# Kernel tuning notes

Measured on AMD Instinct MI355X. Metric: run time of the kernel, lower is better.

The kernel has to match this reference:

```python
import jax, jax.numpy as jnp
import numpy as np

V, C, T, H, L, B = 32000, 1024, 1024, 16, 8, 4
HS = C // H
STD = 0.02


def _layernorm(x, g, b, eps=1e-5):
    m = jnp.mean(x, axis=-1, keepdims=True)
    v = jnp.mean(jnp.square(x - m), axis=-1, keepdims=True)
    return (x - m) * jax.lax.rsqrt(v + eps) * g + b


def setup_inputs() -> dict:
    key = jax.random.key(0)
    ks = jax.random.split(key, 16)
    n = lambda k, shape: (jax.random.normal(k, shape, dtype=jnp.float32) * STD)
    return {
        "index": jax.random.randint(ks[0], (B, T), 0, V),
        "targets": jax.random.randint(ks[1], (B, T), 0, V),
        "tok_emb": n(ks[2], (V, C)),
        "pos_emb": n(ks[3], (T, C)),
        "wq": n(ks[4], (L, C, C)),
        "wk": n(ks[5], (L, C, C)),
        "wv": n(ks[6], (L, C, C)),
        "wo": n(ks[7], (L, C, C)),
        "bo": jnp.zeros((L, C), jnp.float32),
        "w1": n(ks[8], (L, C, 4 * C)),
        "b1": jnp.zeros((L, 4 * C), jnp.float32),
        "w2": n(ks[9], (L, 4 * C, C)),
        "b2": jnp.zeros((L, C), jnp.float32),
        "ln1_g": jnp.ones((L, C), jnp.float32),
        "ln1_b": jnp.zeros((L, C), jnp.float32),
        "ln2_g": jnp.ones((L, C), jnp.float32),
        "ln2_b": jnp.zeros((L, C), jnp.float32),
        "lnf_g": jnp.ones((C,), jnp.float32),
        "lnf_b": jnp.zeros((C,), jnp.float32),
        "lm_w": n(ks[10], (C, V)),
        "lm_b": jnp.zeros((V,), jnp.float32),
    }


def reference(index, targets, tok_emb, pos_emb, wq, wk, wv, wo, bo, w1, b1, w2,
              b2, ln1_g, ln1_b, ln2_g, ln2_b, lnf_g, lnf_b, lm_w, lm_b):
    b, t = index.shape
    x = tok_emb[index] + pos_emb[:t]                      # [B,T,C]
    causal = jnp.tril(jnp.ones((t, t), dtype=bool))       # tril mask
    scale = HS ** -0.5
    for l in range(L):  # fixed small layer loop
        q = (x @ wq[l]).reshape(b, t, H, HS)
        k = (x @ wk[l]).reshape(b, t, H, HS)
        v = (x @ wv[l]).reshape(b, t, H, HS)
        scores = jnp.einsum('bqhd,bkhd->bhqk', q, k) * scale
        scores = jnp.where(causal, scores, -jnp.inf)
        w = jax.nn.softmax(scores, axis=-1)               # dropout p=0 -> identity
        att = jnp.einsum('bhqk,bkhd->bqhd', w, v).reshape(b, t, C)
        x = _layernorm(x + att @ wo[l] + bo[l], ln1_g[l], ln1_b[l])
        h = jax.nn.relu(x @ w1[l] + b1[l])
        x = _layernorm(x + h @ w2[l] + b2[l], ln2_g[l], ln2_b[l])
    x = _layernorm(x, lnf_g, lnf_b)
    logits = (x @ lm_w + lm_b).reshape(b * t, V)
    logp = jax.nn.log_softmax(logits, axis=-1)
    loss = -jnp.take_along_axis(logp, targets.reshape(-1, 1), axis=1).mean()
    return logits, loss
```

## Files before the change

kernel.cpp:

```cpp
#include <hip/hip_runtime.h>

typedef unsigned short u16;
typedef __attribute__((ext_vector_type(4))) float f32x4;
typedef __attribute__((ext_vector_type(8))) short s16x8;
typedef __attribute__((ext_vector_type(4))) short s16x4;

static constexpr int V = 32000;
static constexpr int C = 1024;
static constexpr int T = 1024;
static constexpr int H = 16;
static constexpr int L = 8;
static constexpr int B = 4;
static constexpr int HS = 64;
static constexpr int BT = B * T;
static constexpr int C4 = 4 * C;
static constexpr int C3 = 3 * C;

__device__ __forceinline__ u16 f2bf(float f) {
  union { float f; unsigned u; } v; v.f = f;
  unsigned r = v.u + 0x7fffu + ((v.u >> 16) & 1u);
  return (u16)(r >> 16);
}

__device__ __forceinline__ void gload16(const u16* g, u16* l) {
  __builtin_amdgcn_global_load_lds(
      (const __attribute__((address_space(1))) void*)g,
      (__attribute__((address_space(3))) void*)l, 16, 0, 0);
}

__device__ __forceinline__ float blockReduceSum(float v) {
  __shared__ float red[4];
  int lane = threadIdx.x & 63, w = threadIdx.x >> 6;
#pragma unroll
  for (int m = 32; m >= 1; m >>= 1) v += __shfl_xor(v, m, 64);
  if (lane == 0) red[w] = v;
  __syncthreads();
  float r = red[0] + red[1] + red[2] + red[3];
  __syncthreads();
  return r;
}

__global__ __launch_bounds__(256) void k_embed(
    const int* __restrict__ idx, const float* __restrict__ tok,
    const float* __restrict__ pos, float* __restrict__ x, u16* __restrict__ xb) {
  int bt = blockIdx.x;
  int t = bt & (T - 1);
  int row = idx[bt];
  int tid = threadIdx.x;
  f32x4 tv = ((const f32x4*)(tok + (size_t)row * C))[tid];
  f32x4 pv = ((const f32x4*)(pos + (size_t)t * C))[tid];
  f32x4 y;
  s16x4 yb;
#pragma unroll
  for (int j = 0; j < 4; ++j) {
    y[j] = tv[j] + pv[j];
    yb[j] = (short)f2bf(y[j]);
  }
  ((f32x4*)(x + (size_t)bt * C))[tid] = y;
  ((s16x4*)(xb + (size_t)bt * C))[tid] = yb;
}

__global__ __launch_bounds__(256) void k_transpose(
    const float* __restrict__ W, u16* __restrict__ Wt, int K, int N,
    size_t sW, size_t sWt) {
  __shared__ float tile[64][65];
  const float* Wz = W + sW * blockIdx.z;
  u16* Wtz = Wt + sWt * blockIdx.z;
  int n0 = blockIdx.x * 64, k0 = blockIdx.y * 64;
  int tc = threadIdx.x & 63, tr = threadIdx.x >> 6;
#pragma unroll
  for (int i = 0; i < 16; ++i) {
    int r = tr + i * 4;
    tile[r][tc] = Wz[(size_t)(k0 + r) * N + (n0 + tc)];
  }
  __syncthreads();
#pragma unroll
  for (int i = 0; i < 16; ++i) {
    int r = tr + i * 4;
    Wtz[(size_t)(n0 + r) * K + (k0 + tc)] = f2bf(tile[tc][r]);
  }
}

template <int OUT_BF16, int RELU, int HAS_BIAS, int HAS_RES>
__global__ __launch_bounds__(256, 2) void k_gemm(
    const u16* __restrict__ A, const u16* __restrict__ Bt,
    const float* __restrict__ bias, const float* __restrict__ Res,
    float* __restrict__ Cf, u16* __restrict__ Cb, int M, int N, int K) {
  __shared__ u16 As[3][4096];
  __shared__ u16 Bs[3][4096];
  int tid = threadIdx.x;
  int lane = tid & 63, wid = tid >> 6;
  int lm = lane & 15, lg = lane >> 4;
  int wm = wid >> 1, wn = wid & 1;

  unsigned nbx = gridDim.x;
  unsigned nwg = nbx * gridDim.y;
  unsigned orig = blockIdx.y * nbx + blockIdx.x;
  unsigned f = ((nwg & 7u) == 0u) ? (orig & 7u) * (nwg >> 3) + (orig >> 3) : orig;
  int mb = (int)(f / nbx) * 128, nb = (int)(f % nbx) * 128;

  f32x4 acc[4][4];
#pragma unroll
  for (int i = 0; i < 4; ++i)
#pragma unroll
    for (int j = 0; j < 4; ++j) acc[i][j] = f32x4{0.f, 0.f, 0.f, 0.f};

  int row = tid >> 2, psl = tid & 3;
  int sl = psl ^ (((row & 15) >> 1) & 3);
  const u16* a0 = A + (size_t)(mb + row) * K + sl * 8;
  const u16* a1 = A + (size_t)(mb + 64 + row) * K + sl * 8;
  const u16* b0 = Bt + (size_t)(nb + row) * K + sl * 8;
  const u16* b1 = Bt + (size_t)(nb + 64 + row) * K + sl * 8;
  const int ld0 = wid * 512, ld1 = 2048 + wid * 512;
  const int lo = lm * 32 + ((lg ^ ((lm >> 1) & 3)) << 3);

  auto stage = [&](int t, int s) {
    int ko = t * 32;
    gload16(a0 + ko, &As[s][ld0]);
    gload16(a1 + ko, &As[s][ld1]);
    gload16(b0 + ko, &Bs[s][ld0]);
    gload16(b1 + ko, &Bs[s][ld1]);
  };

  int nK = K >> 5;
  stage(0, 0);
  stage(1, 1);
  for (int t = 0; t < nK; ++t) {
    int s = t % 3;
    if (t + 1 < nK)
      asm volatile("s_waitcnt vmcnt(4)" ::: "memory");
    else
      asm volatile("s_waitcnt vmcnt(0)" ::: "memory");
    __builtin_amdgcn_s_barrier();
    s16x8 af[4], bfr[4];
#pragma unroll
    for (int m = 0; m < 4; ++m)
      af[m] = *(const s16x8*)&As[s][(wm * 4 + m) * 512 + lo];
#pragma unroll
    for (int n = 0; n < 4; ++n)
      bfr[n] = *(const s16x8*)&Bs[s][(wn * 4 + n) * 512 + lo];
    if (t + 2 < nK) stage(t + 2, (t + 2) % 3);
    __builtin_amdgcn_s_setprio(1);
#pragma unroll
    for (int m = 0; m < 4; ++m)
#pragma unroll
      for (int n = 0; n < 4; ++n)
        acc[m][n] = __builtin_amdgcn_mfma_f32_16x16x32_bf16(af[m], bfr[n],
                                                            acc[m][n], 0, 0, 0);
    __builtin_amdgcn_s_setprio(0);
  }
#pragma unroll
  for (int m = 0; m < 4; ++m) {
#pragma unroll
    for (int n = 0; n < 4; ++n) {
      int col = nb + wn * 64 + n * 16 + lm;
      float bv = HAS_BIAS ? bias[col] : 0.0f;
#pragma unroll
      for (int r = 0; r < 4; ++r) {
        int rw = mb + wm * 64 + m * 16 + lg * 4 + r;
        float v = acc[m][n][r] + bv;
        if (HAS_RES) v += Res[(size_t)rw * N + col];
        if (RELU) v = v > 0.f ? v : 0.f;
        if (OUT_BF16)
          Cb[(size_t)rw * N + col] = f2bf(v);
        else
          Cf[(size_t)rw * N + col] = v;
      }
    }
  }
}

template <int OUT_BF16, int RELU, int HAS_BIAS, int HAS_RES, int VT>
__global__ __launch_bounds__(512) void k_gemm256(
    const u16* __restrict__ A, const u16* __restrict__ Bt,
    const float* __restrict__ bias, const float* __restrict__ Res,
    float* __restrict__ Cf, u16* __restrict__ Cb, u16* __restrict__ Vtp,
    int M, int N, int K) {
  __shared__ u16 As[2][16384];
  __shared__ u16 Bs[2][16384];
  const int tid = threadIdx.x;
  const int lane = tid & 63, wid = tid >> 6;
  const int lm = lane & 15, lg = lane >> 4;
  const int wr = wid >> 2, wc = wid & 3;

  unsigned nbx = gridDim.x;
  unsigned nwg = nbx * gridDim.y;
  unsigned orig = blockIdx.y * nbx + blockIdx.x;
  unsigned f =
      ((nwg & 7u) == 0u) ? (orig & 7u) * (nwg >> 3) + (orig >> 3) : orig;
  const int mb = (int)(f / nbx) * 256;
  const int nb = (int)(f % nbx) * 256;

  int aoff[4], boff[4], ldso[4];
#pragma unroll
  for (int h = 0; h < 4; ++h) {
    const int kk = h >> 1, p = h & 1;
    int rem = p * 512 + tid;
    int rblk = rem >> 6;
    int rem2 = rem & 63;
    int row16 = rem2 >> 2, psl = rem2 & 3;
    int sl = psl ^ ((row16 >> 1) & 3);
    int grow = rblk * 16 + row16;
    int gk = kk * 32 + sl * 8;
    aoff[h] = (mb + grow) * K + gk;
    boff[h] = (nb + grow) * K + gk;
    ldso[h] = kk * 8192 + p * 4096 + wid * 512;
  }
  const int lo = lm * 32 + ((lg ^ ((lm >> 1) & 3)) << 3);

  f32x4 acc[8][4];
#pragma unroll
  for (int i = 0; i < 8; ++i)
#pragma unroll
    for (int j = 0; j < 4; ++j) acc[i][j] = f32x4{0.f, 0.f, 0.f, 0.f};

  const int nK = K >> 6;
  gload16(A + aoff[0], &As[0][ldso[0]]);
  gload16(A + aoff[1], &As[0][ldso[1]]);
  gload16(Bt + boff[0], &Bs[0][ldso[0]]);
  gload16(Bt + boff[1], &Bs[0][ldso[1]]);
  gload16(A + aoff[2], &As[0][ldso[2]]);
  gload16(A + aoff[3], &As[0][ldso[3]]);
  gload16(Bt + boff[2], &Bs[0][ldso[2]]);
  gload16(Bt + boff[3], &Bs[0][ldso[3]]);
  asm volatile("s_waitcnt vmcnt(4)" ::: "memory");
  __builtin_amdgcn_s_barrier();

  for (int t = 0; t < nK; ++t) {
    const int buf = t & 1, nbuf = buf ^ 1;
    const bool pre = (t + 1 < nK);
    const int nk64 = (t + 1) * 64;
    s16x8 af[4], bfr[4];
#pragma unroll
    for (int m = 0; m < 4; ++m)
      af[m] = *(const s16x8*)&As[buf][(wr * 8 + m) * 512 + lo];
#pragma unroll
    for (int n = 0; n < 4; ++n)
      bfr[n] = *(const s16x8*)&Bs[buf][(wc * 4 + n) * 512 + lo];
    if (pre) {
      gload16(A + aoff[0] + nk64, &As[nbuf][ldso[0]]);
      gload16(A + aoff[1] + nk64, &As[nbuf][ldso[1]]);
    }
    __builtin_amdgcn_s_barrier();
    __builtin_amdgcn_s_setprio(1);
#pragma unroll
    for (int m = 0; m < 4; ++m)
#pragma unroll
      for (int n = 0; n < 4; ++n)
        acc[m][n] = __builtin_amdgcn_mfma_f32_16x16x32_bf16(af[m], bfr[n],
                                                            acc[m][n], 0, 0, 0);
    __builtin_amdgcn_s_setprio(0);
    __builtin_amdgcn_s_barrier();
#pragma unroll
    for (int m = 0; m < 4; ++m)
      af[m] = *(const s16x8*)&As[buf][(wr * 8 + 4 + m) * 512 + lo];
    if (pre) {
      gload16(Bt + boff[0] + nk64, &Bs[nbuf][ldso[0]]);
      gload16(Bt + boff[1] + nk64, &Bs[nbuf][ldso[1]]);
    }
    __builtin_amdgcn_s_barrier();
    __builtin_amdgcn_s_setprio(1);
#pragma unroll
    for (int m = 0; m < 4; ++m)
#pragma unroll
      for (int n = 0; n < 4; ++n)
        acc[m + 4][n] = __builtin_amdgcn_mfma_f32_16x16x32_bf16(
            af[m], bfr[n], acc[m + 4][n], 0, 0, 0);
    __builtin_amdgcn_s_setprio(0);
    __builtin_amdgcn_s_barrier();
#pragma unroll
    for (int m = 0; m < 4; ++m)
      af[m] = *(const s16x8*)&As[buf][8192 + (wr * 8 + m) * 512 + lo];
#pragma unroll
    for (int n = 0; n < 4; ++n)
      bfr[n] = *(const s16x8*)&Bs[buf][8192 + (wc * 4 + n) * 512 + lo];
    if (pre) {
      gload16(A + aoff[2] + nk64, &As[nbuf][ldso[2]]);
      gload16(A + aoff[3] + nk64, &As[nbuf][ldso[3]]);
      asm volatile("s_waitcnt vmcnt(6)" ::: "memory");
    } else {
      asm volatile("s_waitcnt vmcnt(0)" ::: "memory");
    }
    __builtin_amdgcn_s_barrier();
    __builtin_amdgcn_s_setprio(1);
#pragma unroll
    for (int m = 0; m < 4; ++m)
#pragma unroll
      for (int n = 0; n < 4; ++n)
        acc[m][n] = __builtin_amdgcn_mfma_f32_16x16x32_bf16(af[m], bfr[n],
                                                            acc[m][n], 0, 0, 0);
    __builtin_amdgcn_s_setprio(0);
    __builtin_amdgcn_s_barrier();
#pragma unroll
    for (int m = 0; m < 4; ++m)
      af[m] = *(const s16x8*)&As[buf][8192 + (wr * 8 + 4 + m) * 512 + lo];
    if (pre) {
      gload16(Bt + boff[2] + nk64, &Bs[nbuf][ldso[2]]);
      gload16(Bt + boff[3] + nk64, &Bs[nbuf][ldso[3]]);
      asm volatile("s_waitcnt vmcnt(4)" ::: "memory");
    }
    __builtin_amdgcn_s_barrier();
    __builtin_amdgcn_s_setprio(1);
#pragma unroll
    for (int m = 0; m < 4; ++m)
#pragma unroll
      for (int n = 0; n < 4; ++n)
        acc[m + 4][n] = __builtin_amdgcn_mfma_f32_16x16x32_bf16(
            af[m], bfr[n], acc[m + 4][n], 0, 0, 0);
    __builtin_amdgcn_s_setprio(0);
    __builtin_amdgcn_s_barrier();
  }
  if (VT && nb >= 2 * C) {
    int hh = ((nb - 2 * C) >> 6) + wc;
#pragma unroll
    for (int m = 0; m < 8; ++m) {
      int t0 = mb + wr * 128 + m * 16 + lg * 4;
      int bb = t0 >> 10, tt = t0 & (T - 1);
      size_t vbase = ((size_t)(bb * H + hh) * HS) * T + tt;
#pragma unroll
      for (int n = 0; n < 4; ++n) {
        int d = n * 16 + lm;
        s16x4 pk;
#pragma unroll
        for (int r = 0; r < 4; ++r) pk[r] = (short)f2bf(acc[m][n][r]);
        *(s16x4*)&Vtp[vbase + (size_t)d * T] = pk;
      }
    }
    return;
  }
  float bv[4];
#pragma unroll
  for (int n = 0; n < 4; ++n)
    bv[n] = HAS_BIAS ? bias[nb + wc * 64 + n * 16 + lm] : 0.0f;
#pragma unroll
  for (int m = 0; m < 8; ++m) {
#pragma unroll
    for (int r = 0; r < 4; ++r) {
      int row = mb + wr * 128 + m * 16 + lg * 4 + r;
#pragma unroll
      for (int n = 0; n < 4; ++n) {
        int col = nb + wc * 64 + n * 16 + lm;
        float v = acc[m][n][r] + bv[n];
        if (HAS_RES) v += Res[(size_t)row * N + col];
        if (RELU) v = v > 0.f ? v : 0.f;
        if (OUT_BF16)
          Cb[(size_t)row * N + col] = f2bf(v);
        else
          Cf[(size_t)row * N + col] = v;
      }
    }
  }
}

__global__ __launch_bounds__(1024) void k_lmhead(
    const u16* __restrict__ A, const u16* __restrict__ Bt,
    const float* __restrict__ bias, float* __restrict__ Cf,
    float* __restrict__ Pp, int M, int N, int K) {
  __shared__ u16 As[3][8192];
  __shared__ u16 Bs[3][8192];
  const int tid = threadIdx.x;
  const int lane = tid & 63, wid = tid >> 6;
  const int lm = lane & 15, lg = lane >> 4;
  const int wr = wid >> 2, wc = wid & 3;

  unsigned nbx = gridDim.x;
  unsigned My = gridDim.y;
  unsigned nwg = nbx * My;
  unsigned orig = blockIdx.y * nbx + blockIdx.x;
  unsigned xcd = orig & 7u, idx = orig >> 3;
  unsigned g = xcd * (nwg >> 3) + idx;
  const int mb = (int)(g % My) * 256;
  const int nb = (int)(g / My) * 256;

  int rblk = tid >> 6, rem = tid & 63;
  int row16 = rem >> 2, psl = rem & 3;
  int sl = psl ^ ((row16 >> 1) & 3);
  int grow = rblk * 16 + row16;
  const int aoff = (mb + grow) * K + sl * 8;
  const int boff = (nb + grow) * K + sl * 8;
  const int lds = wid * 512;
  const int lo = lm * 32 + ((lg ^ ((lm >> 1) & 3)) << 3);

  f32x4 acc[4][4];
#pragma unroll
  for (int i = 0; i < 4; ++i)
#pragma unroll
    for (int j = 0; j < 4; ++j) acc[i][j] = f32x4{0.f, 0.f, 0.f, 0.f};

  auto stage = [&](int t, int s) {
    int ko = t * 32;
    gload16(A + aoff + ko, &As[s][lds]);
    gload16(Bt + boff + ko, &Bs[s][lds]);
  };

  const int nK = K >> 5;
  stage(0, 0);
  stage(1, 1);
  for (int t = 0; t < nK; ++t) {
    int s = t % 3;
    if (t + 1 < nK)
      asm volatile("s_waitcnt vmcnt(2)" ::: "memory");
    else
      asm volatile("s_waitcnt vmcnt(0)" ::: "memory");
    __builtin_amdgcn_s_barrier();
    s16x8 af[4], bfr[4];
#pragma unroll
    for (int m = 0; m < 4; ++m)
      af[m] = *(const s16x8*)&As[s][(wr * 4 + m) * 512 + lo];
#pragma unroll
    for (int n = 0; n < 4; ++n)
      bfr[n] = *(const s16x8*)&Bs[s][(wc * 4 + n) * 512 + lo];
    if (t + 2 < nK) stage(t + 2, (t + 2) % 3);
    __builtin_amdgcn_s_setprio(1);
#pragma unroll
    for (int m = 0; m < 4; ++m)
#pragma unroll
      for (int n = 0; n < 4; ++n)
        acc[m][n] = __builtin_amdgcn_mfma_f32_16x16x32_bf16(af[m], bfr[n],
                                                            acc[m][n], 0, 0, 0);
    __builtin_amdgcn_s_setprio(0);
  }
  float bv[4];
#pragma unroll
  for (int n = 0; n < 4; ++n) bv[n] = bias[nb + wc * 64 + n * 16 + lm];
#pragma unroll
  for (int m = 0; m < 4; ++m) {
#pragma unroll
    for (int r = 0; r < 4; ++r) {
      int row = mb + wr * 64 + m * 16 + lg * 4 + r;
#pragma unroll
      for (int n = 0; n < 4; ++n) {
        int col = nb + wc * 64 + n * 16 + lm;
        Cf[(size_t)row * N + col] = acc[m][n][r] + bv[n];
      }
    }
  }
  __syncthreads();
  float* redS = (float*)&As[0][0];
  float Sx[4][4];
#pragma unroll
  for (int m = 0; m < 4; ++m)
#pragma unroll
    for (int r = 0; r < 4; ++r)
      Sx[m][r] = __expf(acc[m][0][r] + bv[0]) + __expf(acc[m][1][r] + bv[1]) +
                 __expf(acc[m][2][r] + bv[2]) + __expf(acc[m][3][r] + bv[3]);
#pragma unroll
  for (int d = 1; d < 16; d <<= 1)
#pragma unroll
    for (int m = 0; m < 4; ++m)
#pragma unroll
      for (int r = 0; r < 4; ++r) Sx[m][r] += __shfl_xor(Sx[m][r], d, 16);
  if (lm == 0) {
#pragma unroll
    for (int m = 0; m < 4; ++m)
#pragma unroll
      for (int r = 0; r < 4; ++r)
        redS[(wr * 64 + m * 16 + lg * 4 + r) * 4 + wc] = Sx[m][r];
  }
  __syncthreads();
  if (tid < 256) {
    float srow = redS[tid * 4 + 0] + redS[tid * 4 + 1] + redS[tid * 4 + 2] +
                 redS[tid * 4 + 3];
    Pp[(size_t)(nb >> 8) * M + mb + tid] = srow;
  }
}

__global__ __launch_bounds__(256) void k_attn(
    const u16* __restrict__ qkv, const u16* __restrict__ vt,
    u16* __restrict__ o) {
  constexpr int PP = 72;
  __shared__ u16 Ks[2][64 * 64];
  __shared__ u16 Vs[2][64 * 64];
  __shared__ u16 Ps[4][16 * PP];
  int bid = blockIdx.x;
  int p = bid & 7, h = (bid >> 3) & 15, b = bid >> 7;
  int tid = threadIdx.x, lane = tid & 63, wid = tid >> 6;
  int lm = lane & 15, lg = lane >> 4;
  const size_t rowbase = (size_t)b * T * C3 + (size_t)h * HS;
  const u16* kbase = qkv + rowbase + C;
  const u16* vbase = vt + (size_t)(b * H + h) * HS * T;
  const size_t obase = (size_t)b * T * C + (size_t)h * HS;
  const float scale = 0.125f;
  const int sr = tid >> 3, scs = (tid & 7) ^ (sr & 7);
  const int swz0 = (lg ^ (lm & 7)) * 8;
  const int swz1 = ((4 + lg) ^ (lm & 7)) * 8;

  for (int qi = 0; qi < 2; ++qi) {
    int qt = qi ? (15 - p) : p;
    int qw = qt * 64 + wid * 16;
    s16x8 qf[2];
#pragma unroll
    for (int s = 0; s < 2; ++s)
      qf[s] = *(const s16x8*)&qkv[rowbase + (size_t)(qw + lm) * C3 + s * 32 +
                                  lg * 8];
    float m_[4], l_[4];
    f32x4 oacc[4];
#pragma unroll
    for (int r = 0; r < 4; ++r) { m_[r] = -3e38f; l_[r] = 0.f; }
#pragma unroll
    for (int n = 0; n < 4; ++n) oacc[n] = f32x4{0.f, 0.f, 0.f, 0.f};

    gload16(kbase + (size_t)sr * C3 + scs * 8, &Ks[0][wid * 512]);
    gload16(kbase + (size_t)(sr + 32) * C3 + scs * 8, &Ks[0][2048 + wid * 512]);
    gload16(vbase + (size_t)sr * T + scs * 8, &Vs[0][wid * 512]);
    gload16(vbase + (size_t)(sr + 32) * T + scs * 8, &Vs[0][2048 + wid * 512]);

    for (int kt = 0; kt <= qt; ++kt) {
      int buf = kt & 1;
      bool pre = kt < qt;
      if (pre) {
        int nk = (kt + 1) * 64;
        int nbuf = buf ^ 1;
        gload16(kbase + (size_t)(nk + sr) * C3 + scs * 8, &Ks[nbuf][wid * 512]);
        gload16(kbase + (size_t)(nk + sr + 32) * C3 + scs * 8,
                &Ks[nbuf][2048 + wid * 512]);
        gload16(vbase + (size_t)sr * T + nk + scs * 8, &Vs[nbuf][wid * 512]);
        gload16(vbase + (size_t)(sr + 32) * T + nk + scs * 8,
                &Vs[nbuf][2048 + wid * 512]);
        asm volatile("s_waitcnt vmcnt(4)" ::: "memory");
      } else {
        asm volatile("s_waitcnt vmcnt(0)" ::: "memory");
      }
      __builtin_amdgcn_s_barrier();

      f32x4 s[4];
#pragma unroll
      for (int ch = 0; ch < 4; ++ch) {
        s16x8 k0 = *(const s16x8*)&Ks[buf][(ch * 16 + lm) * 64 + swz0];
        s16x8 k1 = *(const s16x8*)&Ks[buf][(ch * 16 + lm) * 64 + swz1];
        s[ch] = f32x4{0.f, 0.f, 0.f, 0.f};
        s[ch] = __builtin_amdgcn_mfma_f32_16x16x32_bf16(qf[0], k0, s[ch], 0, 0, 0);
        s[ch] = __builtin_amdgcn_mfma_f32_16x16x32_bf16(qf[1], k1, s[ch], 0, 0, 0);
      }
      if (kt == qt) {
#pragma unroll
        for (int ch = 0; ch < 4; ++ch) {
          int col = kt * 64 + ch * 16 + lm;
#pragma unroll
          for (int r = 0; r < 4; ++r) {
            int row = qw + lg * 4 + r;
            s[ch][r] = (col <= row) ? s[ch][r] * scale : -3e38f;
          }
        }
      } else {
#pragma unroll
        for (int ch = 0; ch < 4; ++ch)
#pragma unroll
          for (int r = 0; r < 4; ++r) s[ch][r] *= scale;
      }
      float rmax[4];
#pragma unroll
      for (int r = 0; r < 4; ++r)
        rmax[r] = fmaxf(fmaxf(s[0][r], s[1][r]), fmaxf(s[2][r], s[3][r]));
#pragma unroll
      for (int mm = 1; mm < 16; mm <<= 1)
#pragma unroll
        for (int r = 0; r < 4; ++r)
          rmax[r] = fmaxf(rmax[r], __shfl_xor(rmax[r], mm, 16));
      float alpha[4], rsum[4];
#pragma unroll
      for (int r = 0; r < 4; ++r) {
        float mn = fmaxf(m_[r], rmax[r]);
        alpha[r] = __expf(m_[r] - mn);
        m_[r] = mn;
        rsum[r] = 0.f;
      }
#pragma unroll
      for (int ch = 0; ch < 4; ++ch)
#pragma unroll
        for (int r = 0; r < 4; ++r) {
          float e = __expf(s[ch][r] - m_[r]);
          s[ch][r] = e;
          rsum[r] += e;
        }
#pragma unroll
      for (int mm = 1; mm < 16; mm <<= 1)
#pragma unroll
        for (int r = 0; r < 4; ++r) rsum[r] += __shfl_xor(rsum[r], mm, 16);
#pragma unroll
      for (int r = 0; r < 4; ++r) l_[r] = l_[r] * alpha[r] + rsum[r];
#pragma unroll
      for (int n = 0; n < 4; ++n)
#pragma unroll
        for (int r = 0; r < 4; ++r) oacc[n][r] *= alpha[r];
#pragma unroll
      for (int r = 0; r < 4; ++r) {
        int pr = lg * 4 + r;
#pragma unroll
        for (int ch = 0; ch < 4; ++ch)
          Ps[wid][pr * PP + ch * 16 + lm] = f2bf(s[ch][r]);
      }
      s16x8 pa0 = *(const s16x8*)&Ps[wid][lm * PP + lg * 8];
      s16x8 pa1 = *(const s16x8*)&Ps[wid][lm * PP + 32 + lg * 8];
#pragma unroll
      for (int n = 0; n < 4; ++n) {
        s16x8 v0 = *(const s16x8*)&Vs[buf][(n * 16 + lm) * 64 + swz0];
        s16x8 v1 = *(const s16x8*)&Vs[buf][(n * 16 + lm) * 64 + swz1];
        oacc[n] =
            __builtin_amdgcn_mfma_f32_16x16x32_bf16(pa0, v0, oacc[n], 0, 0, 0);
        oacc[n] =
            __builtin_amdgcn_mfma_f32_16x16x32_bf16(pa1, v1, oacc[n], 0, 0, 0);
      }
      __builtin_amdgcn_s_barrier();
    }
    float inv[4];
#pragma unroll
    for (int r = 0; r < 4; ++r) inv[r] = 1.0f / l_[r];
#pragma unroll
    for (int n = 0; n < 4; ++n)
#pragma unroll
      for (int r = 0; r < 4; ++r)
        o[obase + (size_t)(qw + lg * 4 + r) * C + n * 16 + lm] =
            f2bf(oacc[n][r] * inv[r]);
  }
}

__global__ __launch_bounds__(256) void k_ln(
    const float* __restrict__ in, const float* __restrict__ g,
    const float* __restrict__ bsh, float* __restrict__ xout,
    u16* __restrict__ xbout) {
  int row = blockIdx.x;
  int tid = threadIdx.x;
  f32x4 v = ((const f32x4*)(in + (size_t)row * C))[tid];
  float s = v[0] + v[1] + v[2] + v[3];
  s = blockReduceSum(s);
  float mean = s * (1.0f / C);
  float s2 = 0.f;
#pragma unroll
  for (int j = 0; j < 4; ++j) {
    float d = v[j] - mean;
    s2 += d * d;
  }
  s2 = blockReduceSum(s2);
  float rstd = rsqrtf(s2 * (1.0f / C) + 1e-5f);
  f32x4 gv = ((const f32x4*)g)[tid];
  f32x4 bv = ((const f32x4*)bsh)[tid];
  f32x4 y;
  s16x4 yb;
#pragma unroll
  for (int j = 0; j < 4; ++j) {
    y[j] = (v[j] - mean) * rstd * gv[j] + bv[j];
    yb[j] = (short)f2bf(y[j]);
  }
  ((f32x4*)(xout + (size_t)row * C))[tid] = y;
  ((s16x4*)(xbout + (size_t)row * C))[tid] = yb;
}

__global__ __launch_bounds__(128) void k_rowloss2(
    const float* __restrict__ sums, const float* __restrict__ logits,
    const int* __restrict__ tgt, float* __restrict__ rowloss) {
  int row = blockIdx.x;
  int tid = threadIdx.x;
  float s = (tid < 125) ? sums[(size_t)tid * BT + row] : 0.f;
#pragma unroll
  for (int d = 1; d < 64; d <<= 1) s += __shfl_xor(s, d, 64);
  __shared__ float ss[2];
  if ((tid & 63) == 0) ss[tid >> 6] = s;
  __syncthreads();
  if (tid == 0)
    rowloss[row] = logf(ss[0] + ss[1]) - logits[(size_t)row * V + tgt[row]];
}

__global__ __launch_bounds__(256) void k_lossreduce(
    const float* __restrict__ rowloss, float* __restrict__ out) {
  __shared__ float red[256];
  int tid = threadIdx.x;
  float s = 0.f;
  for (int i = tid; i < BT; i += 256) s += rowloss[i];
  red[tid] = s;
  __syncthreads();
  for (int m = 128; m >= 1; m >>= 1) {
    if (tid < m) red[tid] += red[tid + m];
    __syncthreads();
  }
  if (tid == 0) out[0] = red[0] * (1.0f / BT);
}

extern "C" void kernel_launch(void* const* d_in, const int* in_sizes, int n_in,
                              void* d_out, int out_size, void* d_ws,
                              size_t ws_size, hipStream_t stream) {
  (void)in_sizes; (void)n_in; (void)out_size; (void)ws_size;
  const int* index = (const int*)d_in[0];
  const int* targets = (const int*)d_in[1];
  const float* tok_emb = (const float*)d_in[2];
  const float* pos_emb = (const float*)d_in[3];
  const float* wq = (const float*)d_in[4];
  const float* wk = (const float*)d_in[5];
  const float* wv = (const float*)d_in[6];
  const float* wo = (const float*)d_in[7];
  const float* bo = (const float*)d_in[8];
  const float* w1 = (const float*)d_in[9];
  const float* b1 = (const float*)d_in[10];
  const float* w2 = (const float*)d_in[11];
  const float* b2 = (const float*)d_in[12];
  const float* ln1_g = (const float*)d_in[13];
  const float* ln1_b = (const float*)d_in[14];
  const float* ln2_g = (const float*)d_in[15];
  const float* ln2_b = (const float*)d_in[16];
  const float* lnf_g = (const float*)d_in[17];
  const float* lnf_b = (const float*)d_in[18];
  const float* lm_w = (const float*)d_in[19];
  const float* lm_b = (const float*)d_in[20];

  float* logits = (float*)d_out;
  float* loss = logits + (size_t)BT * V;

  size_t off = 0;
  auto alloc = [&](size_t bytes) -> void* {
    off = (off + 255) & ~(size_t)255;
    void* p = (void*)((char*)d_ws + off);
    off += bytes;
    return p;
  };
  u16* wqkv_t = (u16*)alloc((size_t)L * C3 * C * 2);
  u16* wo_t = (u16*)alloc((size_t)L * C * C * 2);
  u16* w1_t = (u16*)alloc((size_t)L * C * C4 * 2);
  u16* w2_t = (u16*)alloc((size_t)L * C4 * C * 2);
  u16* lmw_t = (u16*)alloc((size_t)V * C * 2);
  float* x = (float*)alloc((size_t)BT * C * 4);
  float* tmp = (float*)alloc((size_t)BT * C * 4);
  u16* xb = (u16*)alloc((size_t)BT * C * 2);
  u16* qkvb = (u16*)alloc((size_t)BT * C3 * 2);
  u16* vtb = (u16*)alloc((size_t)BT * C * 2);
  u16* attb = (u16*)alloc((size_t)BT * C * 2);
  u16* hb = (u16*)alloc((size_t)BT * C4 * 2);
  float* rowloss = (float*)alloc((size_t)BT * 4);
  float* sums = (float*)alloc((size_t)BT * 128 * 4);

  dim3 blk(256);
  dim3 blk5(512);
  k_transpose<<<dim3(C / 64, C / 64, L), blk, 0, stream>>>(
      wq, wqkv_t, C, C, (size_t)C * C, (size_t)C3 * C);
  k_transpose<<<dim3(C / 64, C / 64, L), blk, 0, stream>>>(
      wk, wqkv_t + (size_t)C * C, C, C, (size_t)C * C, (size_t)C3 * C);
  k_transpose<<<dim3(C / 64, C / 64, L), blk, 0, stream>>>(
      wv, wqkv_t + (size_t)2 * C * C, C, C, (size_t)C * C, (size_t)C3 * C);
  k_transpose<<<dim3(C / 64, C / 64, L), blk, 0, stream>>>(
      wo, wo_t, C, C, (size_t)C * C, (size_t)C * C);
  k_transpose<<<dim3(C4 / 64, C / 64, L), blk, 0, stream>>>(
      w1, w1_t, C, C4, (size_t)C * C4, (size_t)C * C4);
  k_transpose<<<dim3(C / 64, C4 / 64, L), blk, 0, stream>>>(
      w2, w2_t, C4, C, (size_t)C4 * C, (size_t)C4 * C);
  k_transpose<<<dim3(V / 64, C / 64, 1), blk, 0, stream>>>(
      lm_w, lmw_t, C, V, 0, 0);

  k_embed<<<BT, blk, 0, stream>>>(index, tok_emb, pos_emb, x, xb);

  dim3 gQKV(C3 / 256, BT / 256);
  dim3 gCC(C / 128, BT / 128);
  dim3 gC4(C4 / 256, BT / 256);
  for (int l = 0; l < L; ++l) {
    const u16* wqkvt = wqkv_t + (size_t)l * C3 * C;
    const u16* wot = wo_t + (size_t)l * C * C;
    const u16* w1t = w1_t + (size_t)l * C * C4;
    const u16* w2t = w2_t + (size_t)l * C4 * C;

    k_gemm256<1, 0, 0, 0, 1><<<gQKV, blk5, 0, stream>>>(
        xb, wqkvt, nullptr, nullptr, nullptr, qkvb, vtb, BT, C3, C);
    k_attn<<<B * H * 8, blk, 0, stream>>>(qkvb, vtb, attb);
    k_gemm<0, 0, 1, 1><<<gCC, blk, 0, stream>>>(
        attb, wot, bo + (size_t)l * C, x, tmp, nullptr, BT, C, C);
    k_ln<<<BT, blk, 0, stream>>>(tmp, ln1_g + (size_t)l * C,
                                 ln1_b + (size_t)l * C, x, xb);
    k_gemm256<1, 1, 1, 0, 0><<<gC4, blk5, 0, stream>>>(
        xb, w1t, b1 + (size_t)l * C4, nullptr, nullptr, hb, nullptr,
        BT, C4, C);
    k_gemm<0, 0, 1, 1><<<gCC, blk, 0, stream>>>(
        hb, w2t, b2 + (size_t)l * C, x, tmp, nullptr, BT, C, C4);
    k_ln<<<BT, blk, 0, stream>>>(tmp, ln2_g + (size_t)l * C,
                                 ln2_b + (size_t)l * C, x, xb);
  }
  k_ln<<<BT, blk, 0, stream>>>(x, lnf_g, lnf_b, x, xb);
  k_lmhead<<<dim3(V / 256, BT / 256), dim3(1024), 0, stream>>>(
      xb, lmw_t, lm_b, logits, sums, BT, V, C);
  k_rowloss2<<<BT, dim3(128), 0, stream>>>(sums, logits, targets, rowloss);
  k_lossreduce<<<1, blk, 0, stream>>>(rowloss, loss);
}
```

Measured before the change: 2.465 ms.

## Drop 256-tile GEMM for 128-tile GEMM and widen attention KV tile to 128

Removes the 512-thread 256x256 GEMM kernel and routes the QKV and FFN-up GEMMs through the 128x128 triple-buffered kernel, which gains the transposed-V epilogue. The attention kernel now loads 128-key K/V tiles with a single buffer and a full wait per tile instead of double-buffered 64-key tiles, halving loop iterations but giving up load/compute overlap. The smaller GEMM tiles lower per-block data reuse but raise block count and occupancy.

```diff
diff --git a/kernel.cpp b/kernel.cpp
--- a/kernel.cpp
+++ b/kernel.cpp
@@ -81,11 +81,12 @@
   }
 }
 
-template <int OUT_BF16, int RELU, int HAS_BIAS, int HAS_RES>
+template <int OUT_BF16, int RELU, int HAS_BIAS, int HAS_RES, int VT>
 __global__ __launch_bounds__(256, 2) void k_gemm(
     const u16* __restrict__ A, const u16* __restrict__ Bt,
     const float* __restrict__ bias, const float* __restrict__ Res,
-    float* __restrict__ Cf, u16* __restrict__ Cb, int M, int N, int K) {
+    float* __restrict__ Cf, u16* __restrict__ Cb, u16* __restrict__ Vtp,
+    int M, int N, int K) {
   __shared__ u16 As[3][4096];
   __shared__ u16 Bs[3][4096];
   int tid = threadIdx.x;
@@ -149,6 +150,24 @@
                                                             acc[m][n], 0, 0, 0);
     __builtin_amdgcn_s_setprio(0);
   }
+  if (VT && nb >= 2 * C) {
+    int hh = ((nb + wn * 64) - 2 * C) >> 6;
+#pragma unroll
+    for (int m = 0; m < 4; ++m) {
+      int t0 = mb + wm * 64 + m * 16 + lg * 4;
+      int bb = t0 >> 10, tt = t0 & (T - 1);
+      size_t vbase = ((size_t)(bb * H + hh) * HS) * T + tt;
+#pragma unroll
+      for (int n = 0; n < 4; ++n) {
+        int d = n * 16 + lm;
+        s16x4 pk;
+#pragma unroll
+        for (int r = 0; r < 4; ++r) pk[r] = (short)f2bf(acc[m][n][r]);
+        *(s16x4*)&Vtp[vbase + (size_t)d * T] = pk;
+      }
+    }
+    return;
+  }
 #pragma unroll
   for (int m = 0; m < 4; ++m) {
 #pragma unroll
@@ -165,188 +184,6 @@
           Cb[(size_t)rw * N + col] = f2bf(v);
         else
           Cf[(size_t)rw * N + col] = v;
-      }
-    }
-  }
-}
-
-template <int OUT_BF16, int RELU, int HAS_BIAS, int HAS_RES, int VT>
-__global__ __launch_bounds__(512) void k_gemm256(
-    const u16* __restrict__ A, const u16* __restrict__ Bt,
-    const float* __restrict__ bias, const float* __restrict__ Res,
-    float* __restrict__ Cf, u16* __restrict__ Cb, u16* __restrict__ Vtp,
-    int M, int N, int K) {
-  __shared__ u16 As[2][16384];
-  __shared__ u16 Bs[2][16384];
-  const int tid = threadIdx.x;
-  const int lane = tid & 63, wid = tid >> 6;
-  const int lm = lane & 15, lg = lane >> 4;
-  const int wr = wid >> 2, wc = wid & 3;
-
-  unsigned nbx = gridDim.x;
-  unsigned nwg = nbx * gridDim.y;
-  unsigned orig = blockIdx.y * nbx + blockIdx.x;
-  unsigned f =
-      ((nwg & 7u) == 0u) ? (orig & 7u) * (nwg >> 3) + (orig >> 3) : orig;
-  const int mb = (int)(f / nbx) * 256;
-  const int nb = (int)(f % nbx) * 256;
-
-  int aoff[4], boff[4], ldso[4];
-#pragma unroll
-  for (int h = 0; h < 4; ++h) {
-    const int kk = h >> 1, p = h & 1;
-    int rem = p * 512 + tid;
-    int rblk = rem >> 6;
-    int rem2 = rem & 63;
-    int row16 = rem2 >> 2, psl = rem2 & 3;
-    int sl = psl ^ ((row16 >> 1) & 3);
-    int grow = rblk * 16 + row16;
-    int gk = kk * 32 + sl * 8;
-    aoff[h] = (mb + grow) * K + gk;
-    boff[h] = (nb + grow) * K + gk;
-    ldso[h] = kk * 8192 + p * 4096 + wid * 512;
-  }
-  const int lo = lm * 32 + ((lg ^ ((lm >> 1) & 3)) << 3);
-
-  f32x4 acc[8][4];
-#pragma unroll
-  for (int i = 0; i < 8; ++i)
-#pragma unroll
-    for (int j = 0; j < 4; ++j) acc[i][j] = f32x4{0.f, 0.f, 0.f, 0.f};
-
-  const int nK = K >> 6;
-  gload16(A + aoff[0], &As[0][ldso[0]]);
-  gload16(A + aoff[1], &As[0][ldso[1]]);
-  gload16(Bt + boff[0], &Bs[0][ldso[0]]);
-  gload16(Bt + boff[1], &Bs[0][ldso[1]]);
-  gload16(A + aoff[2], &As[0][ldso[2]]);
-  gload16(A + aoff[3], &As[0][ldso[3]]);
-  gload16(Bt + boff[2], &Bs[0][ldso[2]]);
-  gload16(Bt + boff[3], &Bs[0][ldso[3]]);
-  asm volatile("s_waitcnt vmcnt(4)" ::: "memory");
-  __builtin_amdgcn_s_barrier();
-
-  for (int t = 0; t < nK; ++t) {
-    const int buf = t & 1, nbuf = buf ^ 1;
-    const bool pre = (t + 1 < nK);
-    const int nk64 = (t + 1) * 64;
-    s16x8 af[4], bfr[4];
-#pragma unroll
-    for (int m = 0; m < 4; ++m)
-      af[m] = *(const s16x8*)&As[buf][(wr * 8 + m) * 512 + lo];
-#pragma unroll
-    for (int n = 0; n < 4; ++n)
-      bfr[n] = *(const s16x8*)&Bs[buf][(wc * 4 + n) * 512 + lo];
-    if (pre) {
-      gload16(A + aoff[0] + nk64, &As[nbuf][ldso[0]]);
-      gload16(A + aoff[1] + nk64, &As[nbuf][ldso[1]]);
-    }
-    __builtin_amdgcn_s_barrier();
-    __builtin_amdgcn_s_setprio(1);
-#pragma unroll
-    for (int m = 0; m < 4; ++m)
-#pragma unroll
-      for (int n = 0; n < 4; ++n)
-        acc[m][n] = __builtin_amdgcn_mfma_f32_16x16x32_bf16(af[m], bfr[n],
-                                                            acc[m][n], 0, 0, 0);
-    __builtin_amdgcn_s_setprio(0);
-    __builtin_amdgcn_s_barrier();
-#pragma unroll
-    for (int m = 0; m < 4; ++m)
-      af[m] = *(const s16x8*)&As[buf][(wr * 8 + 4 + m) * 512 + lo];
-    if (pre) {
-      gload16(Bt + boff[0] + nk64, &Bs[nbuf][ldso[0]]);
-      gload16(Bt + boff[1] + nk64, &Bs[nbuf][ldso[1]]);
-    }
-    __builtin_amdgcn_s_barrier();
-    __builtin_amdgcn_s_setprio(1);
-#pragma unroll
-    for (int m = 0; m < 4; ++m)
-#pragma unroll
-      for (int n = 0; n < 4; ++n)
-        acc[m + 4][n] = __builtin_amdgcn_mfma_f32_16x16x32_bf16(
-            af[m], bfr[n], acc[m + 4][n], 0, 0, 0);
-    __builtin_amdgcn_s_setprio(0);
-    __builtin_amdgcn_s_barrier();
-#pragma unroll
-    for (int m = 0; m < 4; ++m)
-      af[m] = *(const s16x8*)&As[buf][8192 + (wr * 8 + m) * 512 + lo];
-#pragma unroll
-    for (int n = 0; n < 4; ++n)
-      bfr[n] = *(const s16x8*)&Bs[buf][8192 + (wc * 4 + n) * 512 + lo];
-    if (pre) {
-      gload16(A + aoff[2] + nk64, &As[nbuf][ldso[2]]);
-      gload16(A + aoff[3] + nk64, &As[nbuf][ldso[3]]);
-      asm volatile("s_waitcnt vmcnt(6)" ::: "memory");
-    } else {
-      asm volatile("s_waitcnt vmcnt(0)" ::: "memory");
-    }
-    __builtin_amdgcn_s_barrier();
-    __builtin_amdgcn_s_setprio(1);
-#pragma unroll
-    for (int m = 0; m < 4; ++m)
-#pragma unroll
-      for (int n = 0; n < 4; ++n)
-        acc[m][n] = __builtin_amdgcn_mfma_f32_16x16x32_bf16(af[m], bfr[n],
-                                                            acc[m][n], 0, 0, 0);
-    __builtin_amdgcn_s_setprio(0);
-    __builtin_amdgcn_s_barrier();
-#pragma unroll
-    for (int m = 0; m < 4; ++m)
-      af[m] = *(const s16x8*)&As[buf][8192 + (wr * 8 + 4 + m) * 512 + lo];
-    if (pre) {
-      gload16(Bt + boff[2] + nk64, &Bs[nbuf][ldso[2]]);
-      gload16(Bt + boff[3] + nk64, &Bs[nbuf][ldso[3]]);
-      asm volatile("s_waitcnt vmcnt(4)" ::: "memory");
-    }
-    __builtin_amdgcn_s_barrier();
-    __builtin_amdgcn_s_setprio(1);
-#pragma unroll
-    for (int m = 0; m < 4; ++m)
-#pragma unroll
-      for (int n = 0; n < 4; ++n)
-        acc[m + 4][n] = __builtin_amdgcn_mfma_f32_16x16x32_bf16(
-            af[m], bfr[n], acc[m + 4][n], 0, 0, 0);
-    __builtin_amdgcn_s_setprio(0);
-    __builtin_amdgcn_s_barrier();
-  }
-  if (VT && nb >= 2 * C) {
-    int hh = ((nb - 2 * C) >> 6) + wc;
-#pragma unroll
-    for (int m = 0; m < 8; ++m) {
-      int t0 = mb + wr * 128 + m * 16 + lg * 4;
-      int bb = t0 >> 10, tt = t0 & (T - 1);
-      size_t vbase = ((size_t)(bb * H + hh) * HS) * T + tt;
-#pragma unroll
-      for (int n = 0; n < 4; ++n) {
-        int d = n * 16 + lm;
-        s16x4 pk;
-#pragma unroll
-        for (int r = 0; r < 4; ++r) pk[r] = (short)f2bf(acc[m][n][r]);
-        *(s16x4*)&Vtp[vbase + (size_t)d * T] = pk;
-      }
-    }
-    return;
-  }
-  float bv[4];
-#pragma unroll
-  for (int n = 0; n < 4; ++n)
-    bv[n] = HAS_BIAS ? bias[nb + wc * 64 + n * 16 + lm] : 0.0f;
-#pragma unroll
-  for (int m = 0; m < 8; ++m) {
-#pragma unroll
-    for (int r = 0; r < 4; ++r) {
-      int row = mb + wr * 128 + m * 16 + lg * 4 + r;
-#pragma unroll
-      for (int n = 0; n < 4; ++n) {
-        int col = nb + wc * 64 + n * 16 + lm;
-        float v = acc[m][n][r] + bv[n];
-        if (HAS_RES) v += Res[(size_t)row * N + col];
-        if (RELU) v = v > 0.f ? v : 0.f;
-        if (OUT_BF16)
-          Cb[(size_t)row * N + col] = f2bf(v);
-        else
-          Cf[(size_t)row * N + col] = v;
       }
     }
   }
@@ -468,9 +305,9 @@
 __global__ __launch_bounds__(256) void k_attn(
     const u16* __restrict__ qkv, const u16* __restrict__ vt,
     u16* __restrict__ o) {
-  constexpr int PP = 72;
-  __shared__ u16 Ks[2][64 * 64];
-  __shared__ u16 Vs[2][64 * 64];
+  constexpr int PP = 136;
+  __shared__ u16 Ks[128 * 64];
+  __shared__ u16 Vs[64 * 128];
   __shared__ u16 Ps[4][16 * PP];
   int bid = blockIdx.x;
   int p = bid & 7, h = (bid >> 3) & 15, b = bid >> 7;
@@ -481,9 +318,17 @@
   const u16* vbase = vt + (size_t)(b * H + h) * HS * T;
   const size_t obase = (size_t)b * T * C + (size_t)h * HS;
   const float scale = 0.125f;
-  const int sr = tid >> 3, scs = (tid & 7) ^ (sr & 7);
-  const int swz0 = (lg ^ (lm & 7)) * 8;
-  const int swz1 = ((4 + lg) ^ (lm & 7)) * 8;
+  const int ksr = tid >> 3, kcs = (tid & 7) ^ (ksr & 7);
+  const int vsr = tid >> 4, vc0 = tid & 15;
+  const int vcs = (vc0 & 8) | ((vc0 & 7) ^ (vsr & 7));
+  const int swzk0 = (lg ^ (lm & 7)) * 8;
+  const int swzk1 = ((4 + lg) ^ (lm & 7)) * 8;
+  int vsw[4];
+#pragma unroll
+  for (int g = 0; g < 2 * 2; ++g) {
+    int c = g * 4 + lg;
+    vsw[g] = ((c & 8) | ((c & 7) ^ (lm & 7))) * 8;
+  }
 
   for (int qi = 0; qi < 2; ++qi) {
     int qt = qi ? (15 - p) : p;
@@ -500,42 +345,33 @@
 #pragma unroll
     for (int n = 0; n < 4; ++n) oacc[n] = f32x4{0.f, 0.f, 0.f, 0.f};
 
-    gload16(kbase + (size_t)sr * C3 + scs * 8, &Ks[0][wid * 512]);
-    gload16(kbase + (size_t)(sr + 32) * C3 + scs * 8, &Ks[0][2048 + wid * 512]);
-    gload16(vbase + (size_t)sr * T + scs * 8, &Vs[0][wid * 512]);
-    gload16(vbase + (size_t)(sr + 32) * T + scs * 8, &Vs[0][2048 + wid * 512]);
-
-    for (int kt = 0; kt <= qt; ++kt) {
-      int buf = kt & 1;
-      bool pre = kt < qt;
-      if (pre) {
-        int nk = (kt + 1) * 64;
-        int nbuf = buf ^ 1;
-        gload16(kbase + (size_t)(nk + sr) * C3 + scs * 8, &Ks[nbuf][wid * 512]);
-        gload16(kbase + (size_t)(nk + sr + 32) * C3 + scs * 8,
-                &Ks[nbuf][2048 + wid * 512]);
-        gload16(vbase + (size_t)sr * T + nk + scs * 8, &Vs[nbuf][wid * 512]);
-        gload16(vbase + (size_t)(sr + 32) * T + nk + scs * 8,
-                &Vs[nbuf][2048 + wid * 512]);
-        asm volatile("s_waitcnt vmcnt(4)" ::: "memory");
-      } else {
-        asm volatile("s_waitcnt vmcnt(0)" ::: "memory");
-      }
+    const int nkt = (qt + 2) >> 1;
+    for (int kt = 0; kt < nkt; ++kt) {
+      __syncthreads();
+#pragma unroll
+      for (int j = 0; j < 4; ++j)
+        gload16(kbase + (size_t)(kt * 128 + j * 32 + ksr) * C3 + kcs * 8,
+                &Ks[j * 2048 + wid * 512]);
+#pragma unroll
+      for (int j = 0; j < 4; ++j)
+        gload16(vbase + (size_t)(j * 16 + vsr) * T + kt * 128 + vcs * 8,
+                &Vs[j * 2048 + wid * 512]);
+      asm volatile("s_waitcnt vmcnt(0)" ::: "memory");
       __builtin_amdgcn_s_barrier();
 
-      f32x4 s[4];
-#pragma unroll
-      for (int ch = 0; ch < 4; ++ch) {
-        s16x8 k0 = *(const s16x8*)&Ks[buf][(ch * 16 + lm) * 64 + swz0];
-        s16x8 k1 = *(const s16x8*)&Ks[buf][(ch * 16 + lm) * 64 + swz1];
+      f32x4 s[8];
+#pragma unroll
+      for (int ch = 0; ch < 8; ++ch) {
+        s16x8 k0 = *(const s16x8*)&Ks[(ch * 16 + lm) * 64 + swzk0];
+        s16x8 k1 = *(const s16x8*)&Ks[(ch * 16 + lm) * 64 + swzk1];
         s[ch] = f32x4{0.f, 0.f, 0.f, 0.f};
         s[ch] = __builtin_amdgcn_mfma_f32_16x16x32_bf16(qf[0], k0, s[ch], 0, 0, 0);
         s[ch] = __builtin_amdgcn_mfma_f32_16x16x32_bf16(qf[1], k1, s[ch], 0, 0, 0);
       }
-      if (kt == qt) {
-#pragma unroll
-        for (int ch = 0; ch < 4; ++ch) {
-          int col = kt * 64 + ch * 16 + lm;
+      if (kt == nkt - 1) {
+#pragma unroll
+        for (int ch = 0; ch < 8; ++ch) {
+          int col = kt * 128 + ch * 16 + lm;
 #pragma unroll
           for (int r = 0; r < 4; ++r) {
             int row = qw + lg * 4 + r;
@@ -544,14 +380,17 @@
         }
       } else {
 #pragma unroll
-        for (int ch = 0; ch < 4; ++ch)
+        for (int ch = 0; ch < 8; ++ch)
 #pragma unroll
           for (int r = 0; r < 4; ++r) s[ch][r] *= scale;
       }
       float rmax[4];
 #pragma unroll
-      for (int r = 0; r < 4; ++r)
-        rmax[r] = fmaxf(fmaxf(s[0][r], s[1][r]), fmaxf(s[2][r], s[3][r]));
+      for (int r = 0; r < 4; ++r) {
+        float a = fmaxf(fmaxf(s[0][r], s[1][r]), fmaxf(s[2][r], s[3][r]));
+        float bb2 = fmaxf(fmaxf(s[4][r], s[5][r]), fmaxf(s[6][r], s[7][r]));
+        rmax[r] = fmaxf(a, bb2);
+      }
 #pragma unroll
       for (int mm = 1; mm < 16; mm <<= 1)
 #pragma unroll
@@ -566,7 +405,7 @@
         rsum[r] = 0.f;
       }
 #pragma unroll
-      for (int ch = 0; ch < 4; ++ch)
+      for (int ch = 0; ch < 8; ++ch)
 #pragma unroll
         for (int r = 0; r < 4; ++r) {
           float e = __expf(s[ch][r] - m_[r]);
@@ -587,21 +426,22 @@
       for (int r = 0; r < 4; ++r) {
         int pr = lg * 4 + r;
 #pragma unroll
-        for (int ch = 0; ch < 4; ++ch)
+        for (int ch = 0; ch < 8; ++ch)
           Ps[wid][pr * PP + ch * 16 + lm] = f2bf(s[ch][r]);
       }
-      s16x8 pa0 = *(const s16x8*)&Ps[wid][lm * PP + lg * 8];
-      s16x8 pa1 = *(const s16x8*)&Ps[wid][lm * PP + 32 + lg * 8];
+      s16x8 pa[4];
+#pragma unroll
+      for (int g = 0; g < 4; ++g)
+        pa[g] = *(const s16x8*)&Ps[wid][lm * PP + g * 32 + lg * 8];
 #pragma unroll
       for (int n = 0; n < 4; ++n) {
-        s16x8 v0 = *(const s16x8*)&Vs[buf][(n * 16 + lm) * 64 + swz0];
-        s16x8 v1 = *(const s16x8*)&Vs[buf][(n * 16 + lm) * 64 + swz1];
-        oacc[n] =
-            __builtin_amdgcn_mfma_f32_16x16x32_bf16(pa0, v0, oacc[n], 0, 0, 0);
-        oacc[n] =
-            __builtin_amdgcn_mfma_f32_16x16x32_bf16(pa1, v1, oacc[n], 0, 0, 0);
-      }
-      __builtin_amdgcn_s_barrier();
+#pragma unroll
+        for (int g = 0; g < 4; ++g) {
+          s16x8 vf = *(const s16x8*)&Vs[(n * 16 + lm) * 128 + vsw[g]];
+          oacc[n] = __builtin_amdgcn_mfma_f32_16x16x32_bf16(pa[g], vf,
+                                                            oacc[n], 0, 0, 0);
+        }
+      }
     }
     float inv[4];
 #pragma unroll
@@ -728,7 +568,6 @@
   float* sums = (float*)alloc((size_t)BT * 128 * 4);
 
   dim3 blk(256);
-  dim3 blk5(512);
   k_transpose<<<dim3(C / 64, C / 64, L), blk, 0, stream>>>(
       wq, wqkv_t, C, C, (size_t)C * C, (size_t)C3 * C);
   k_transpose<<<dim3(C / 64, C / 64, L), blk, 0, stream>>>(
@@ -746,27 +585,27 @@
 
   k_embed<<<BT, blk, 0, stream>>>(index, tok_emb, pos_emb, x, xb);
 
-  dim3 gQKV(C3 / 256, BT / 256);
+  dim3 gQKV(C3 / 128, BT / 128);
   dim3 gCC(C / 128, BT / 128);
-  dim3 gC4(C4 / 256, BT / 256);
+  dim3 gC4(C4 / 128, BT / 128);
   for (int l = 0; l < L; ++l) {
     const u16* wqkvt = wqkv_t + (size_t)l * C3 * C;
     const u16* wot = wo_t + (size_t)l * C * C;
     const u16* w1t = w1_t + (size_t)l * C * C4;
     const u16* w2t = w2_t + (size_t)l * C4 * C;
 
-    k_gemm256<1, 0, 0, 0, 1><<<gQKV, blk5, 0, stream>>>(
+    k_gemm<1, 0, 0, 0, 1><<<gQKV, blk, 0, stream>>>(
         xb, wqkvt, nullptr, nullptr, nullptr, qkvb, vtb, BT, C3, C);
     k_attn<<<B * H * 8, blk, 0, stream>>>(qkvb, vtb, attb);
-    k_gemm<0, 0, 1, 1><<<gCC, blk, 0, stream>>>(
-        attb, wot, bo + (size_t)l * C, x, tmp, nullptr, BT, C, C);
+    k_gemm<0, 0, 1, 1, 0><<<gCC, blk, 0, stream>>>(
+        attb, wot, bo + (size_t)l * C, x, tmp, nullptr, nullptr, BT, C, C);
     k_ln<<<BT, blk, 0, stream>>>(tmp, ln1_g + (size_t)l * C,
                                  ln1_b + (size_t)l * C, x, xb);
-    k_gemm256<1, 1, 1, 0, 0><<<gC4, blk5, 0, stream>>>(
+    k_gemm<1, 1, 1, 0, 0><<<gC4, blk, 0, stream>>>(
         xb, w1t, b1 + (size_t)l * C4, nullptr, nullptr, hb, nullptr,
         BT, C4, C);
-    k_gemm<0, 0, 1, 1><<<gCC, blk, 0, stream>>>(
-        hb, w2t, b2 + (size_t)l * C, x, tmp, nullptr, BT, C, C4);
+    k_gemm<0, 0, 1, 1, 0><<<gCC, blk, 0, stream>>>(
+        hb, w2t, b2 + (size_t)l * C, x, tmp, nullptr, nullptr, BT, C, C4);
     k_ln<<<BT, blk, 0, stream>>>(tmp, ln2_g + (size_t)l * C,
                                  ln2_b + (size_t)l * C, x, xb);
   }
```

Result: slower. 2.520 ms (+2.2%).
